# Performance work log

Hardware: AMD Instinct MI355X
Metric: run time of the kernel (lower is better)

Reference implementation:

```python
import jax, jax.numpy as jnp
import numpy as np
from jax.scipy.special import gammaln, xlogy

B, S, C = 2, 2048, 1536
H, DK, DV = 8, 64, 192
F_REL = C // H  # 192 relative-position features


def positional_features_all(positions, feature_size, seq_length):
    # positions: [1, 2S-1] float32 (signed relative distances)
    n = feature_size // 6  # basis per class per sign
    ap = jnp.abs(positions)  # [1, 2S-1]
    Sf = float(seq_length)
    # exponential decay features
    max_range = float(np.log(Sf) / np.log(2.0))
    half_life = 2.0 ** jnp.linspace(3.0, max_range, n)  # min_half_life = 3.0
    feat_exp = jnp.exp(-jnp.log(2.0) / half_life * ap[..., None])
    # central mask features
    center_widths = 2.0 ** jnp.arange(1, n + 1, dtype=jnp.float32) - 1.0
    feat_cm = (center_widths > ap[..., None]).astype(jnp.float32)
    # gamma pdf features
    stddev = Sf / (2.0 * n)
    start_mean = Sf / n
    mean = jnp.linspace(start_mean, Sf, n)
    conc = (mean / stddev) ** 2
    rate = mean / (stddev ** 2)
    xg = ap[..., None]
    log_unnorm = xlogy(conc - 1.0, xg) - rate * xg
    log_norm = gammaln(conc) - conc * jnp.log(rate)
    prob = jnp.exp(log_unnorm - log_norm) + 1e-8
    feat_g = prob / jnp.max(prob, axis=1, keepdims=True)
    emb = jnp.concatenate([feat_exp, feat_cm, feat_g], axis=-1)  # [1, 2S-1, 3n]
    emb = jnp.concatenate([emb, jnp.sign(positions)[..., None] * emb], axis=-1)
    return emb  # [1, 2S-1, feature_size]


def relative_shift(x):
    # x: [B, H, T, 2T-1] -> [B, H, T, T] (Transformer-XL shift trick)
    b, h, t, _ = x.shape
    x = jnp.pad(x, ((0, 0), (0, 0), (0, 0), (1, 0)))  # [B,H,T,2T]
    x = x.reshape(b, h, 2 * t, t)[:, :, 1:, :]          # [B,H,2T-1,T]
    x = x.reshape(b, h, t, 2 * t - 1)[:, :, :, :t]      # [B,H,T,T]
    return x


def setup_inputs() -> dict:
    key = jax.random.key(0)
    ks = jax.random.split(key, 8)
    inp = {
        "x": jax.random.normal(ks[0], (B, S, C), dtype=jnp.float32),
        "mask": jax.random.randint(ks[1], (B, S), 0, 2, dtype=jnp.int32),
        "Wq": jax.random.normal(ks[2], (C, H * DK), dtype=jnp.float32) * 0.02,
        "Wk": jax.random.normal(ks[3], (C, H * DK), dtype=jnp.float32) * 0.02,
        "Wv": jax.random.normal(ks[4], (C, H * DV), dtype=jnp.float32) * 0.02,
        "Wr": jax.random.normal(ks[5], (F_REL, H * DK), dtype=jnp.float32) * 0.02,
        "r_w_bias": jax.random.normal(ks[6], (1, H, 1, DK), dtype=jnp.float32) * 0.02,
        "Wo": jax.random.normal(ks[7], (H * DV, H * DV), dtype=jnp.float32) * 0.02,
        "bo": jnp.zeros((H * DV,), dtype=jnp.float32),
    }
    return inp


def reference(x, mask, Wq, Wk, Wv, Wr, r_w_bias, Wo, bo):
    b, s, c = x.shape
    # projections -> [B, H, S, d]
    q = (x @ Wq).reshape(b, s, H, DK).transpose(0, 2, 1, 3) * (DK ** -0.5)
    k = (x @ Wk).reshape(b, s, H, DK).transpose(0, 2, 1, 3)
    v = (x @ Wv).reshape(b, s, H, DV).transpose(0, 2, 1, 3)
    # relative positional encodings for distances -S+1 .. S-1
    dist = jnp.arange(-s + 1, s, dtype=jnp.float32)[None, :]  # [1, 2S-1]
    pe = positional_features_all(dist, F_REL, s)               # [1, 2S-1, F_REL]
    r_k = (pe[0] @ Wr).reshape(2 * s - 1, H, DK).transpose(1, 0, 2)  # [H, 2S-1, DK]
    # content + position logits
    content_logits = jnp.einsum('bhqd,bhkd->bhqk', q, k)                   # [B,H,S,S]
    rel_logits = jnp.einsum('bhqd,hkd->bhqk', q + r_w_bias, r_k)           # [B,H,S,2S-1]
    logits = content_logits + relative_shift(rel_logits)
    logits = jnp.where(mask[:, None, None, :] == 0, -1e9, logits)
    weights = jax.nn.softmax(logits, axis=-1)
    out = jnp.einsum('bhqk,bhkd->bhqd', weights, v)  # [B,H,S,DV]
    out = out.transpose(0, 2, 1, 3).reshape(b, s, H * DV)
    return out @ Wo + bo
```

## Files before the change

### kernel.cpp

```cpp
#include <hip/hip_runtime.h>
#include <math.h>

#define SEQ 2048
#define CDIM 1536
#define HN 8
#define DVC 192
#define BN 2
#define NPOS 4095
#define HDK 512
#define HDV 1536
#define PSTR 72

typedef __attribute__((ext_vector_type(8))) _Float16 hf8v;
typedef __attribute__((ext_vector_type(4))) _Float16 hf4v;
typedef __attribute__((ext_vector_type(4))) float f4v;

static __device__ __forceinline__ f4v mfma16(hf8v a, hf8v b, f4v c) {
  return __builtin_amdgcn_mfma_f32_16x16x32_f16(a, b, c, 0, 0, 0);
}
static __device__ __forceinline__ void gl2lds16(const void* g, void* l) {
  __builtin_amdgcn_global_load_lds((const __attribute__((address_space(1))) unsigned int*)g,
                                   (__attribute__((address_space(3))) unsigned int*)l,
                                   16, 0, 0);
}
static __device__ __forceinline__ float rowmax16(float x) {
  x = fmaxf(x, __int_as_float(__builtin_amdgcn_update_dpp(0, __float_as_int(x), 0x128, 0xf, 0xf, true)));
  x = fmaxf(x, __int_as_float(__builtin_amdgcn_update_dpp(0, __float_as_int(x), 0x124, 0xf, 0xf, true)));
  x = fmaxf(x, __int_as_float(__builtin_amdgcn_update_dpp(0, __float_as_int(x), 0x122, 0xf, 0xf, true)));
  x = fmaxf(x, __int_as_float(__builtin_amdgcn_update_dpp(0, __float_as_int(x), 0x121, 0xf, 0xf, true)));
  return x;
}

#define PF_B   512
#define CAST_B 6144
#define TWQ_B  768
#define TWK_B  768
#define TWV_B  2304
#define TWO_B  2304
#define TWR_B  96
#define PREP_BLOCKS (PF_B + CAST_B + TWQ_B + TWK_B + TWV_B + TWO_B + TWR_B)

__device__ __forceinline__ void twc_tile(const float* __restrict__ W, _Float16* __restrict__ WT,
                                         int K, int N, int tile, float (*tls)[33], int tid) {
  int ntn = N >> 5;
  int nt = tile % ntn, kt = tile / ntn;
  int k0 = kt * 32, n0 = nt * 32;
  int tx = tid & 31, ty = tid >> 5;
#pragma unroll
  for (int p = 0; p < 4; p++) tls[ty + p * 8][tx] = W[(size_t)(k0 + ty + p * 8) * N + n0 + tx];
  __syncthreads();
#pragma unroll
  for (int p = 0; p < 4; p++) {
    int n = ty + p * 8;
    WT[(size_t)(n0 + n) * K + k0 + tx] = (_Float16)tls[tx][n];
  }
}

__global__ __launch_bounds__(256) void prep_kernel(
    const float* __restrict__ x, const float* __restrict__ Wq, const float* __restrict__ Wk,
    const float* __restrict__ Wv, const float* __restrict__ Wo, const float* __restrict__ Wr,
    float* __restrict__ pe_raw, unsigned* __restrict__ gmax, _Float16* __restrict__ xb,
    _Float16* __restrict__ WTqkv, _Float16* __restrict__ WoT, _Float16* __restrict__ WrT) {
  __shared__ float tls[32][33];
  int blk = blockIdx.x, tid = threadIdx.x;
  if (blk < PF_B) {
    int j = blk >> 4;
    int pos = (blk & 15) * 256 + tid;
    float prob = 0.0f;
    if (pos < NPOS) {
      float ap = fabsf((float)(pos - (SEQ - 1)));
      float hl = exp2f(3.0f + 8.0f * (float)j / 31.0f);
      float fe = exp2f(-ap / hl);
      float cw = exp2f((float)(j + 1)) - 1.0f;
      float fc = (cw > ap) ? 1.0f : 0.0f;
      float conc = 4.0f * (float)((j + 1) * (j + 1));
      float rate = (float)(j + 1) / 16.0f;
      float log_norm = lgammaf(conc) - conc * logf(rate);
      float log_un = (conc - 1.0f) * logf(ap) - rate * ap;
      prob = expf(log_un - log_norm) + 1e-8f;
      pe_raw[pos * 96 + j] = fe;
      pe_raw[pos * 96 + 32 + j] = fc;
      pe_raw[pos * 96 + 64 + j] = prob;
    }
    float m = prob;
#pragma unroll
    for (int off = 32; off > 0; off >>= 1) m = fmaxf(m, __shfl_down(m, off));
    __shared__ float red[4];
    if ((tid & 63) == 0) red[tid >> 6] = m;
    __syncthreads();
    if (tid == 0) {
      m = fmaxf(fmaxf(red[0], red[1]), fmaxf(red[2], red[3]));
      atomicMax(&gmax[j], __float_as_uint(m));
    }
  } else if (blk < PF_B + CAST_B) {
    int i = ((blk - PF_B) * 256 + tid) * 4;
    float4 v = *(const float4*)(x + i);
    _Float16 o[4] = {(_Float16)v.x, (_Float16)v.y, (_Float16)v.z, (_Float16)v.w};
    *(unsigned long long*)(xb + i) = *(const unsigned long long*)o;
  } else if (blk < PF_B + CAST_B + TWQ_B) {
    twc_tile(Wq, WTqkv + 0 * (size_t)CDIM, CDIM, HDK, blk - (PF_B + CAST_B), tls, tid);
  } else if (blk < PF_B + CAST_B + TWQ_B + TWK_B) {
    twc_tile(Wk, WTqkv + 512 * (size_t)CDIM, CDIM, HDK, blk - (PF_B + CAST_B + TWQ_B), tls, tid);
  } else if (blk < PF_B + CAST_B + TWQ_B + TWK_B + TWV_B) {
    twc_tile(Wv, WTqkv + 1024 * (size_t)CDIM, CDIM, HDV, blk - (PF_B + CAST_B + TWQ_B + TWK_B), tls, tid);
  } else if (blk < PF_B + CAST_B + TWQ_B + TWK_B + TWV_B + TWO_B) {
    twc_tile(Wo, WoT, CDIM, HDV, blk - (PF_B + CAST_B + TWQ_B + TWK_B + TWV_B), tls, tid);
  } else {
    twc_tile(Wr, WrT, 192, HDK, blk - (PF_B + CAST_B + TWQ_B + TWK_B + TWV_B + TWO_B), tls, tid);
  }
}

__global__ __launch_bounds__(256) void pe_norm_kernel(const float* __restrict__ pe_raw,
                                                      const unsigned* __restrict__ gmax,
                                                      _Float16* __restrict__ pe_h) {
  int idx = blockIdx.x * 256 + threadIdx.x;
  int pos = idx / 96, f = idx - pos * 96;
  float val = 0.0f, sval = 0.0f;
  if (pos < NPOS) {
    val = pe_raw[pos * 96 + f];
    if (f >= 64) val *= 1.0f / __uint_as_float(gmax[f - 64]);
    float sgn = (pos > SEQ - 1) ? 1.0f : ((pos < SEQ - 1) ? -1.0f : 0.0f);
    sval = sgn * val;
  }
  pe_h[pos * 192 + f] = (_Float16)val;
  pe_h[pos * 192 + 96 + f] = (_Float16)sval;
}

template <int MODE>
__global__ __launch_bounds__(256, 2) void mfma_gemm(
    const _Float16* __restrict__ A, const _Float16* __restrict__ B,
    const float* __restrict__ bias, void* __restrict__ out0, void* __restrict__ out1,
    void* __restrict__ out2, int K) {
  __shared__ __align__(16) _Float16 As[128 * 64];
  __shared__ __align__(16) _Float16 Bs[128 * 64];
  const int tid = threadIdx.x;
  const int lane = tid & 63, l15 = lane & 15, quad = lane >> 4;
  const int wv = tid >> 6;
  const int wm = (wv & 1) * 64, wn = (wv >> 1) * 64;
  const int row0 = blockIdx.y * 128, col0 = blockIdx.x * 128;
  f4v acc[4][4];
#pragma unroll
  for (int i = 0; i < 4; i++)
#pragma unroll
    for (int j = 0; j < 4; j++) acc[i][j] = (f4v)0.0f;

  for (int k0 = 0; k0 < K; k0 += 64) {
    __syncthreads();
#pragma unroll
    for (int p = 0; p < 4; p++) {
      int idx = tid + p * 256;
      int rr = idx >> 3, sc = idx & 7;
      int gc = (sc ^ (rr & 7)) << 3;
      gl2lds16(A + (size_t)(row0 + rr) * K + k0 + gc, As + idx * 8);
      gl2lds16(B + (size_t)(col0 + rr) * K + k0 + gc, Bs + idx * 8);
    }
    __syncthreads();
    hf8v af[4][2], bfr[4][2];
#pragma unroll
    for (int t = 0; t < 4; t++) {
      int lrA = wm + t * 16 + l15;
      int lrB = wn + t * 16 + l15;
#pragma unroll
      for (int kc = 0; kc < 2; kc++) {
        af[t][kc]  = *(const hf8v*)(As + lrA * 64 + ((((kc << 2) | quad) ^ (lrA & 7)) << 3));
        bfr[t][kc] = *(const hf8v*)(Bs + lrB * 64 + ((((kc << 2) | quad) ^ (lrB & 7)) << 3));
      }
    }
#pragma unroll
    for (int kc = 0; kc < 2; kc++)
#pragma unroll
      for (int mt = 0; mt < 4; mt++)
#pragma unroll
        for (int nt = 0; nt < 4; nt++)
          acc[mt][nt] = mfma16(af[mt][kc], bfr[nt][kc], acc[mt][nt]);
  }
#pragma unroll
  for (int mt = 0; mt < 4; mt++)
#pragma unroll
    for (int reg = 0; reg < 4; reg++) {
      int r = row0 + wm + mt * 16 + quad * 4 + reg;
      int bb = r >> 11, ss = r & (SEQ - 1);
#pragma unroll
      for (int nt = 0; nt < 4; nt++) {
        int c = col0 + wn + nt * 16 + l15;
        float vv = acc[mt][nt][reg];
        if (MODE == 0) {
          if (c < 512) {
            ((_Float16*)out0)[(size_t)r * HDK + c] = (_Float16)(vv * 0.125f);
          } else if (c < 1024) {
            int cc = c - 512, h = cc >> 6, d = cc & 63;
            ((_Float16*)out1)[(((size_t)bb * HN + h) * SEQ + ss) * 64 + d] = (_Float16)vv;
          } else {
            int cc = c - 1024, h = cc / DVC, e = cc - h * DVC;
            int jp = (ss & ~63) | ((ss & 15) << 2) | ((ss >> 4) & 3);
            ((_Float16*)out2)[(((size_t)bb * HN + h) * DVC + e) * SEQ + jp] = (_Float16)vv;
          }
        } else if (MODE == 1) {
          int h = c >> 6, d = c & 63;
          ((_Float16*)out0)[((size_t)h * 4096 + r) * 64 + d] = (_Float16)vv;
        } else {
          ((float*)out0)[(size_t)r * HDV + c] = vv + bias[c];
        }
      }
    }
}

template <bool SPLITKV>
__global__ __launch_bounds__(256, 2) void attn_mfma(
    const _Float16* __restrict__ qb, const _Float16* __restrict__ kb,
    const _Float16* __restrict__ vtb, const _Float16* __restrict__ rkb,
    const float* __restrict__ rwb, const int* __restrict__ mask,
    _Float16* __restrict__ attn_out, float* __restrict__ Opart, float* __restrict__ ml) {
  __shared__ __align__(16) _Float16 Vts[192 * 64];
  __shared__ __align__(16) _Float16 RKs[192 * 64];
  __shared__ __align__(16) _Float16 Kts[64 * 64];
  __shared__ __align__(16) _Float16 Pbs[128 * PSTR];

  const int lin = blockIdx.x;
  const int chunk = SPLITKV ? 64 : 32;
  const int swz = (lin & 7) * chunk + (lin >> 3);
  const int bx = swz & 15;
  const int by = swz >> 4;
  const int i0 = bx * 128;
  const int bh = SPLITKV ? (by & 15) : by;
  const int half = SPLITKV ? (by >> 4) : 0;
  const int b = bh >> 3, h = bh & 7;
  const int tid = threadIdx.x;
  const int wv = tid >> 6, lane = tid & 63;
  const int l15 = lane & 15, quad = lane >> 4;

  hf8v qf[2][2], qbf[2][2];
#pragma unroll
  for (int s = 0; s < 2; s++) {
    int qrow = i0 + wv * 32 + s * 16 + l15;
    const _Float16* qp = qb + (size_t)(b * SEQ + qrow) * HDK + h * 64;
#pragma unroll
    for (int kc = 0; kc < 2; kc++) {
      hf8v qv = *(const hf8v*)(qp + kc * 32 + quad * 8);
      qf[s][kc] = qv;
      hf8v t;
#pragma unroll
      for (int j = 0; j < 8; j++)
        t[j] = (_Float16)((float)qv[j] + rwb[h * 64 + kc * 32 + quad * 8 + j]);
      qbf[s][kc] = t;
    }
  }

  f4v Of[2][12];
#pragma unroll
  for (int s = 0; s < 2; s++)
#pragma unroll
    for (int se = 0; se < 12; se++) Of[s][se] = (f4v)0.0f;
  float m_i[2][4] = {{-INFINITY, -INFINITY, -INFINITY, -INFINITY},
                     {-INFINITY, -INFINITY, -INFINITY, -INFINITY}};
  float l_i[2][4] = {{0.f, 0.f, 0.f, 0.f}, {0.f, 0.f, 0.f, 0.f}};

  const int j0beg = SPLITKV ? half * (SEQ / 2) : 0;
  const int j0end = SPLITKV ? j0beg + SEQ / 2 : SEQ;

  for (int j0 = j0beg; j0 < j0end; j0 += 64) {
    __syncthreads();
    int mraw[4];
#pragma unroll
    for (int st = 0; st < 4; st++) mraw[st] = mask[b * SEQ + j0 + st * 16 + l15];
    {
      const int U0 = j0 - i0 + 1920;
#pragma unroll
      for (int r = 0; r < 2; r++) {
        int idx = tid + r * 256, row = idx >> 3, sc = idx & 7;
        gl2lds16(kb + ((size_t)bh * SEQ + j0 + row) * 64 + ((sc ^ (row & 7)) << 3), Kts + idx * 8);
      }
#pragma unroll
      for (int r = 0; r < 6; r++) {
        int idx = tid + r * 256, row = idx >> 3, sc = idx & 7;
        gl2lds16(rkb + ((size_t)h * 4096 + U0 + row) * 64 + ((sc ^ (row & 7)) << 3), RKs + idx * 8);
      }
#pragma unroll
      for (int r = 0; r < 6; r++) {
        int idx = tid + r * 256, row = idx >> 3, sc = idx & 7;
        gl2lds16(vtb + ((size_t)bh * DVC + row) * SEQ + j0 + ((sc ^ (row & 7)) << 3), Vts + idx * 8);
      }
    }
    asm volatile("s_waitcnt vmcnt(6)" ::: "memory");
    __builtin_amdgcn_s_barrier();
    __builtin_amdgcn_sched_barrier(0);
    float mv[4];
#pragma unroll
    for (int st = 0; st < 4; st++) mv[st] = mraw[st] ? 0.f : -1e9f;

#pragma unroll
    for (int s = 0; s < 2; s++) {
      __builtin_amdgcn_s_setprio(1);
      f4v Sf[4];
#pragma unroll
      for (int st = 0; st < 4; st++) {
        Sf[st] = (f4v)0.0f;
#pragma unroll
        for (int kc = 0; kc < 2; kc++) {
          int row = st * 16 + l15;
          hf8v kf = *(const hf8v*)(Kts + row * 64 + ((((kc << 2) | quad) ^ (row & 7)) << 3));
          Sf[st] = mfma16(qf[s][kc], kf, Sf[st]);
        }
      }
      f4v Rf[5];
      const int tb = 112 - 32 * wv - 16 * s;
#pragma unroll
      for (int u = 0; u < 5; u++) {
        Rf[u] = (f4v)0.0f;
#pragma unroll
        for (int kc = 0; kc < 2; kc++) {
          int row = tb + u * 16 + l15;
          hf8v rf = *(const hf8v*)(RKs + row * 64 + ((((kc << 2) | quad) ^ (row & 7)) << 3));
          Rf[u] = mfma16(qbf[s][kc], rf, Rf[u]);
        }
      }
      __builtin_amdgcn_s_setprio(0);
#pragma unroll
      for (int reg = 0; reg < 4; reg++) {
        int delta = l15 - (quad << 2) - reg + 15;
        int srcl = (quad << 4) | (delta & 15);
        float sh0 = __shfl(Rf[0][reg], srcl, 64);
        float sh1 = __shfl(Rf[1][reg], srcl, 64);
        float sh2 = __shfl(Rf[2][reg], srcl, 64);
        float sh3 = __shfl(Rf[3][reg], srcl, 64);
        float sh4 = __shfl(Rf[4][reg], srcl, 64);
        bool hib = delta >= 16;
        Sf[0][reg] += (hib ? sh1 : sh0) + mv[0];
        Sf[1][reg] += (hib ? sh2 : sh1) + mv[1];
        Sf[2][reg] += (hib ? sh3 : sh2) + mv[2];
        Sf[3][reg] += (hib ? sh4 : sh3) + mv[3];
      }
#pragma unroll
      for (int reg = 0; reg < 4; reg++) {
        float t = fmaxf(fmaxf(Sf[0][reg], Sf[1][reg]), fmaxf(Sf[2][reg], Sf[3][reg]));
        t = rowmax16(t);
        if (__any(t - m_i[s][reg] > 8.0f)) {
          float mn = fmaxf(m_i[s][reg], t);
          float alpha = __expf(m_i[s][reg] - mn);
          m_i[s][reg] = mn;
          l_i[s][reg] *= alpha;
#pragma unroll
          for (int se = 0; se < 12; se++) Of[s][se][reg] *= alpha;
        }
        float mcur = m_i[s][reg];
        hf4v pv;
        float rs = 0.f;
#pragma unroll
        for (int st = 0; st < 4; st++) {
          float p = __expf(Sf[st][reg] - mcur);
          rs += p;
          pv[st] = (_Float16)p;
        }
        l_i[s][reg] += rs;
        *(hf4v*)(Pbs + (size_t)(wv * 32 + s * 16 + quad * 4 + reg) * PSTR + l15 * 4) = pv;
      }
    }

    hf8v pa[2][2];
#pragma unroll
    for (int s = 0; s < 2; s++)
#pragma unroll
      for (int kc = 0; kc < 2; kc++)
        pa[s][kc] = *(const hf8v*)(Pbs + (size_t)(wv * 32 + s * 16 + l15) * PSTR +
                                   kc * 32 + quad * 8);
    asm volatile("s_waitcnt vmcnt(0)" ::: "memory");
    __builtin_amdgcn_s_barrier();
    __builtin_amdgcn_sched_barrier(0);
    __builtin_amdgcn_s_setprio(1);
#pragma unroll
    for (int se = 0; se < 12; se++) {
#pragma unroll
      for (int kc = 0; kc < 2; kc++) {
        int row = se * 16 + l15;
        hf8v vf = *(const hf8v*)(Vts + row * 64 + ((((kc << 2) | quad) ^ (row & 7)) << 3));
        Of[0][se] = mfma16(pa[0][kc], vf, Of[0][se]);
        Of[1][se] = mfma16(pa[1][kc], vf, Of[1][se]);
      }
    }
    __builtin_amdgcn_s_setprio(0);
  }

#pragma unroll
  for (int s = 0; s < 2; s++)
#pragma unroll
    for (int reg = 0; reg < 4; reg++) {
      float ls = l_i[s][reg];
      ls += __shfl_xor(ls, 1);
      ls += __shfl_xor(ls, 2);
      ls += __shfl_xor(ls, 4);
      ls += __shfl_xor(ls, 8);
      int row = i0 + wv * 32 + s * 16 + quad * 4 + reg;
      int rg = b * SEQ + row;
      if constexpr (SPLITKV) {
        float* Op = Opart + ((size_t)(half * 4096 + rg)) * HDV + h * DVC;
#pragma unroll
        for (int se = 0; se < 12; se++) Op[se * 16 + l15] = Of[s][se][reg];
        if (l15 == 0) {
          size_t mlb = (((size_t)half * 4096 + rg) * HN + h) * 2;
          ml[mlb] = m_i[s][reg];
          ml[mlb + 1] = ls;
        }
      } else {
        float inv = 1.0f / ls;
        size_t base2 = (size_t)rg * HDV + h * DVC;
#pragma unroll
        for (int se = 0; se < 12; se++)
          attn_out[base2 + se * 16 + l15] = (_Float16)(Of[s][se][reg] * inv);
      }
    }
}

__global__ __launch_bounds__(256) void combine_kernel(const float* __restrict__ Opart,
                                                      const float* __restrict__ ml,
                                                      _Float16* __restrict__ attn_out) {
  int i4 = blockIdx.x * 256 + threadIdx.x;
  int rg = i4 / 384, c4 = (i4 - rg * 384) * 4;
  int h = c4 / DVC;
  size_t mlb0 = ((size_t)rg * HN + h) * 2;
  size_t mlb1 = (((size_t)4096 + rg) * HN + h) * 2;
  float m0 = ml[mlb0], l0 = ml[mlb0 + 1];
  float m1 = ml[mlb1], l1 = ml[mlb1 + 1];
  float M = fmaxf(m0, m1);
  float w0 = __expf(m0 - M), w1 = __expf(m1 - M);
  float inv = 1.0f / (l0 * w0 + l1 * w1);
  float4 O0 = *(const float4*)(Opart + (size_t)rg * HDV + c4);
  float4 O1 = *(const float4*)(Opart + ((size_t)4096 + rg) * HDV + c4);
  _Float16 o[4] = {(_Float16)((O0.x * w0 + O1.x * w1) * inv),
                   (_Float16)((O0.y * w0 + O1.y * w1) * inv),
                   (_Float16)((O0.z * w0 + O1.z * w1) * inv),
                   (_Float16)((O0.w * w0 + O1.w * w1) * inv)};
  *(unsigned long long*)(attn_out + (size_t)rg * HDV + c4) = *(const unsigned long long*)o;
}

extern "C" void kernel_launch(void* const* d_in, const int* in_sizes, int n_in,
                              void* d_out, int out_size, void* d_ws, size_t ws_size,
                              hipStream_t stream) {
  const float* x    = (const float*)d_in[0];
  const int*   mask = (const int*)d_in[1];
  const float* Wq   = (const float*)d_in[2];
  const float* Wk   = (const float*)d_in[3];
  const float* Wv   = (const float*)d_in[4];
  const float* Wr   = (const float*)d_in[5];
  const float* rwb  = (const float*)d_in[6];
  const float* Wo   = (const float*)d_in[7];
  const float* bo   = (const float*)d_in[8];
  float* out = (float*)d_out;

  char* wsb = (char*)d_ws;
  size_t o = 0;
  auto al = [](size_t v) { return (v + 255) & ~(size_t)255; };
#define CARVE(ptr_t, name, bytes) ptr_t name = (ptr_t)(wsb + o); o = al(o + (bytes));
  CARVE(float*, pe_raw, (size_t)4096 * 96 * 4)
  CARVE(unsigned*, gmax, 128)
  CARVE(_Float16*, pe_h, (size_t)4096 * 192 * 2)
  CARVE(_Float16*, WrT, (size_t)HDK * 192 * 2)
  CARVE(_Float16*, xb, (size_t)BN * SEQ * CDIM * 2)
  CARVE(_Float16*, WTqkv, (size_t)2560 * CDIM * 2)
  CARVE(_Float16*, WoT, (size_t)HDV * CDIM * 2)
  CARVE(_Float16*, qb, (size_t)BN * SEQ * HDK * 2)
  CARVE(_Float16*, kb, (size_t)BN * SEQ * HDK * 2)
  CARVE(_Float16*, vtb, (size_t)BN * SEQ * HDV * 2)
  CARVE(_Float16*, rkb, (size_t)HN * 4096 * 64 * 2)
  _Float16* attnh = xb;
  CARVE(float*, Opart, (size_t)2 * 4096 * HDV * 4)
  CARVE(float*, ml, (size_t)2 * 4096 * HN * 2 * 4)
  bool dosplit = (o <= ws_size);

  hipMemsetAsync(gmax, 0, 32 * sizeof(unsigned), stream);
  prep_kernel<<<PREP_BLOCKS, 256, 0, stream>>>(x, Wq, Wk, Wv, Wo, Wr, pe_raw, gmax, xb,
                                               WTqkv, WoT, WrT);
  pe_norm_kernel<<<4096 * 96 / 256, 256, 0, stream>>>(pe_raw, gmax, pe_h);
  mfma_gemm<0><<<dim3(2560 / 128, BN * SEQ / 128), 256, 0, stream>>>(
      xb, WTqkv, nullptr, qb, kb, vtb, CDIM);
  mfma_gemm<1><<<dim3(HDK / 128, 4096 / 128), 256, 0, stream>>>(
      pe_h, WrT, nullptr, rkb, nullptr, nullptr, 192);
  if (dosplit) {
    attn_mfma<true><<<512, 256, 0, stream>>>(qb, kb, vtb, rkb, rwb, mask,
                                             attnh, Opart, ml);
    combine_kernel<<<4096 * 384 / 256, 256, 0, stream>>>(Opart, ml, attnh);
  } else {
    attn_mfma<false><<<256, 256, 0, stream>>>(qb, kb, vtb, rkb, rwb, mask,
                                              attnh, nullptr, nullptr);
  }
  mfma_gemm<2><<<dim3(HDV / 128, BN * SEQ / 128), 256, 0, stream>>>(
      attnh, WoT, bo, out, nullptr, nullptr, CDIM);
}
```

Before: 316.8 us.

## Split attention block into 8 waves with 16 query rows each

The attention kernel now runs 512 threads (8 waves) per block instead of 256. Each wave handles 16 query rows instead of 32, so per-thread accumulator and Q registers are halved, and the K/RK/V tile loads are shared across twice as many threads. The aim is more resident waves and better latency hiding. In exchange each V and RK fragment read from LDS feeds only one MFMA instead of two, which raises LDS traffic per FLOP, and barriers now synchronise more waves.

```diff
diff --git a/kernel.cpp b/kernel.cpp
--- a/kernel.cpp
+++ b/kernel.cpp
@@ -206,7 +206,7 @@
 }
 
 template <bool SPLITKV>
-__global__ __launch_bounds__(256, 2) void attn_mfma(
+__global__ __launch_bounds__(512, 4) void attn_mfma(
     const _Float16* __restrict__ qb, const _Float16* __restrict__ kb,
     const _Float16* __restrict__ vtb, const _Float16* __restrict__ rkb,
     const float* __restrict__ rwb, const int* __restrict__ mask,
@@ -229,31 +229,27 @@
   const int wv = tid >> 6, lane = tid & 63;
   const int l15 = lane & 15, quad = lane >> 4;
 
-  hf8v qf[2][2], qbf[2][2];
-#pragma unroll
-  for (int s = 0; s < 2; s++) {
-    int qrow = i0 + wv * 32 + s * 16 + l15;
+  hf8v qf[2], qbf[2];
+  {
+    int qrow = i0 + wv * 16 + l15;
     const _Float16* qp = qb + (size_t)(b * SEQ + qrow) * HDK + h * 64;
 #pragma unroll
     for (int kc = 0; kc < 2; kc++) {
       hf8v qv = *(const hf8v*)(qp + kc * 32 + quad * 8);
-      qf[s][kc] = qv;
+      qf[kc] = qv;
       hf8v t;
 #pragma unroll
       for (int j = 0; j < 8; j++)
         t[j] = (_Float16)((float)qv[j] + rwb[h * 64 + kc * 32 + quad * 8 + j]);
-      qbf[s][kc] = t;
-    }
-  }
-
-  f4v Of[2][12];
-#pragma unroll
-  for (int s = 0; s < 2; s++)
-#pragma unroll
-    for (int se = 0; se < 12; se++) Of[s][se] = (f4v)0.0f;
-  float m_i[2][4] = {{-INFINITY, -INFINITY, -INFINITY, -INFINITY},
-                     {-INFINITY, -INFINITY, -INFINITY, -INFINITY}};
-  float l_i[2][4] = {{0.f, 0.f, 0.f, 0.f}, {0.f, 0.f, 0.f, 0.f}};
+      qbf[kc] = t;
+    }
+  }
+
+  f4v Of[12];
+#pragma unroll
+  for (int se = 0; se < 12; se++) Of[se] = (f4v)0.0f;
+  float m_i[4] = {-INFINITY, -INFINITY, -INFINITY, -INFINITY};
+  float l_i[4] = {0.f, 0.f, 0.f, 0.f};
 
   const int j0beg = SPLITKV ? half * (SEQ / 2) : 0;
   const int j0end = SPLITKV ? j0beg + SEQ / 2 : SEQ;
@@ -265,104 +261,97 @@
     for (int st = 0; st < 4; st++) mraw[st] = mask[b * SEQ + j0 + st * 16 + l15];
     {
       const int U0 = j0 - i0 + 1920;
-#pragma unroll
-      for (int r = 0; r < 2; r++) {
-        int idx = tid + r * 256, row = idx >> 3, sc = idx & 7;
-        gl2lds16(kb + ((size_t)bh * SEQ + j0 + row) * 64 + ((sc ^ (row & 7)) << 3), Kts + idx * 8);
-      }
-#pragma unroll
-      for (int r = 0; r < 6; r++) {
-        int idx = tid + r * 256, row = idx >> 3, sc = idx & 7;
+      {
+        int row = tid >> 3, sc = tid & 7;
+        gl2lds16(kb + ((size_t)bh * SEQ + j0 + row) * 64 + ((sc ^ (row & 7)) << 3), Kts + tid * 8);
+      }
+#pragma unroll
+      for (int r = 0; r < 3; r++) {
+        int idx = tid + r * 512, row = idx >> 3, sc = idx & 7;
         gl2lds16(rkb + ((size_t)h * 4096 + U0 + row) * 64 + ((sc ^ (row & 7)) << 3), RKs + idx * 8);
       }
 #pragma unroll
-      for (int r = 0; r < 6; r++) {
-        int idx = tid + r * 256, row = idx >> 3, sc = idx & 7;
+      for (int r = 0; r < 3; r++) {
+        int idx = tid + r * 512, row = idx >> 3, sc = idx & 7;
         gl2lds16(vtb + ((size_t)bh * DVC + row) * SEQ + j0 + ((sc ^ (row & 7)) << 3), Vts + idx * 8);
       }
     }
-    asm volatile("s_waitcnt vmcnt(6)" ::: "memory");
+    asm volatile("s_waitcnt vmcnt(3)" ::: "memory");
     __builtin_amdgcn_s_barrier();
     __builtin_amdgcn_sched_barrier(0);
     float mv[4];
 #pragma unroll
     for (int st = 0; st < 4; st++) mv[st] = mraw[st] ? 0.f : -1e9f;
 
-#pragma unroll
-    for (int s = 0; s < 2; s++) {
-      __builtin_amdgcn_s_setprio(1);
-      f4v Sf[4];
+    __builtin_amdgcn_s_setprio(1);
+    f4v Sf[4];
+#pragma unroll
+    for (int st = 0; st < 4; st++) {
+      Sf[st] = (f4v)0.0f;
+#pragma unroll
+      for (int kc = 0; kc < 2; kc++) {
+        int row = st * 16 + l15;
+        hf8v kf = *(const hf8v*)(Kts + row * 64 + ((((kc << 2) | quad) ^ (row & 7)) << 3));
+        Sf[st] = mfma16(qf[kc], kf, Sf[st]);
+      }
+    }
+    f4v Rf[5];
+    const int tb = 112 - 16 * wv;
+#pragma unroll
+    for (int u = 0; u < 5; u++) {
+      Rf[u] = (f4v)0.0f;
+#pragma unroll
+      for (int kc = 0; kc < 2; kc++) {
+        int row = tb + u * 16 + l15;
+        hf8v rf = *(const hf8v*)(RKs + row * 64 + ((((kc << 2) | quad) ^ (row & 7)) << 3));
+        Rf[u] = mfma16(qbf[kc], rf, Rf[u]);
+      }
+    }
+    __builtin_amdgcn_s_setprio(0);
+#pragma unroll
+    for (int reg = 0; reg < 4; reg++) {
+      int delta = l15 - (quad << 2) - reg + 15;
+      int srcl = (quad << 4) | (delta & 15);
+      float sh0 = __shfl(Rf[0][reg], srcl, 64);
+      float sh1 = __shfl(Rf[1][reg], srcl, 64);
+      float sh2 = __shfl(Rf[2][reg], srcl, 64);
+      float sh3 = __shfl(Rf[3][reg], srcl, 64);
+      float sh4 = __shfl(Rf[4][reg], srcl, 64);
+      bool hib = delta >= 16;
+      Sf[0][reg] += (hib ? sh1 : sh0) + mv[0];
+      Sf[1][reg] += (hib ? sh2 : sh1) + mv[1];
+      Sf[2][reg] += (hib ? sh3 : sh2) + mv[2];
+      Sf[3][reg] += (hib ? sh4 : sh3) + mv[3];
+    }
+#pragma unroll
+    for (int reg = 0; reg < 4; reg++) {
+      float t = fmaxf(fmaxf(Sf[0][reg], Sf[1][reg]), fmaxf(Sf[2][reg], Sf[3][reg]));
+      t = rowmax16(t);
+      if (__any(t - m_i[reg] > 8.0f)) {
+        float mn = fmaxf(m_i[reg], t);
+        float alpha = __expf(m_i[reg] - mn);
+        m_i[reg] = mn;
+        l_i[reg] *= alpha;
+#pragma unroll
+        for (int se = 0; se < 12; se++) Of[se][reg] *= alpha;
+      }
+      float mcur = m_i[reg];
+      hf4v pv;
+      float rs = 0.f;
 #pragma unroll
       for (int st = 0; st < 4; st++) {
-        Sf[st] = (f4v)0.0f;
-#pragma unroll
-        for (int kc = 0; kc < 2; kc++) {
-          int row = st * 16 + l15;
-          hf8v kf = *(const hf8v*)(Kts + row * 64 + ((((kc << 2) | quad) ^ (row & 7)) << 3));
-          Sf[st] = mfma16(qf[s][kc], kf, Sf[st]);
-        }
-      }
-      f4v Rf[5];
-      const int tb = 112 - 32 * wv - 16 * s;
-#pragma unroll
-      for (int u = 0; u < 5; u++) {
-        Rf[u] = (f4v)0.0f;
-#pragma unroll
-        for (int kc = 0; kc < 2; kc++) {
-          int row = tb + u * 16 + l15;
-          hf8v rf = *(const hf8v*)(RKs + row * 64 + ((((kc << 2) | quad) ^ (row & 7)) << 3));
-          Rf[u] = mfma16(qbf[s][kc], rf, Rf[u]);
-        }
-      }
-      __builtin_amdgcn_s_setprio(0);
-#pragma unroll
-      for (int reg = 0; reg < 4; reg++) {
-        int delta = l15 - (quad << 2) - reg + 15;
-        int srcl = (quad << 4) | (delta & 15);
-        float sh0 = __shfl(Rf[0][reg], srcl, 64);
-        float sh1 = __shfl(Rf[1][reg], srcl, 64);
-        float sh2 = __shfl(Rf[2][reg], srcl, 64);
-        float sh3 = __shfl(Rf[3][reg], srcl, 64);
-        float sh4 = __shfl(Rf[4][reg], srcl, 64);
-        bool hib = delta >= 16;
-        Sf[0][reg] += (hib ? sh1 : sh0) + mv[0];
-        Sf[1][reg] += (hib ? sh2 : sh1) + mv[1];
-        Sf[2][reg] += (hib ? sh3 : sh2) + mv[2];
-        Sf[3][reg] += (hib ? sh4 : sh3) + mv[3];
-      }
-#pragma unroll
-      for (int reg = 0; reg < 4; reg++) {
-        float t = fmaxf(fmaxf(Sf[0][reg], Sf[1][reg]), fmaxf(Sf[2][reg], Sf[3][reg]));
-        t = rowmax16(t);
-        if (__any(t - m_i[s][reg] > 8.0f)) {
-          float mn = fmaxf(m_i[s][reg], t);
-          float alpha = __expf(m_i[s][reg] - mn);
-          m_i[s][reg] = mn;
-          l_i[s][reg] *= alpha;
-#pragma unroll
-          for (int se = 0; se < 12; se++) Of[s][se][reg] *= alpha;
-        }
-        float mcur = m_i[s][reg];
-        hf4v pv;
-        float rs = 0.f;
-#pragma unroll
-        for (int st = 0; st < 4; st++) {
-          float p = __expf(Sf[st][reg] - mcur);
-          rs += p;
-          pv[st] = (_Float16)p;
-        }
-        l_i[s][reg] += rs;
-        *(hf4v*)(Pbs + (size_t)(wv * 32 + s * 16 + quad * 4 + reg) * PSTR + l15 * 4) = pv;
-      }
-    }
-
-    hf8v pa[2][2];
-#pragma unroll
-    for (int s = 0; s < 2; s++)
-#pragma unroll
-      for (int kc = 0; kc < 2; kc++)
-        pa[s][kc] = *(const hf8v*)(Pbs + (size_t)(wv * 32 + s * 16 + l15) * PSTR +
-                                   kc * 32 + quad * 8);
+        float p = __expf(Sf[st][reg] - mcur);
+        rs += p;
+        pv[st] = (_Float16)p;
+      }
+      l_i[reg] += rs;
+      *(hf4v*)(Pbs + (size_t)(wv * 16 + quad * 4 + reg) * PSTR + l15 * 4) = pv;
+    }
+
+    hf8v pa[2];
+#pragma unroll
+    for (int kc = 0; kc < 2; kc++)
+      pa[kc] = *(const hf8v*)(Pbs + (size_t)(wv * 16 + l15) * PSTR + kc * 32 + quad * 8);
     asm volatile("s_waitcnt vmcnt(0)" ::: "memory");
     __builtin_amdgcn_s_barrier();
     __builtin_amdgcn_sched_barrier(0);
@@ -373,41 +362,38 @@
       for (int kc = 0; kc < 2; kc++) {
         int row = se * 16 + l15;
         hf8v vf = *(const hf8v*)(Vts + row * 64 + ((((kc << 2) | quad) ^ (row & 7)) << 3));
-        Of[0][se] = mfma16(pa[0][kc], vf, Of[0][se]);
-        Of[1][se] = mfma16(pa[1][kc], vf, Of[1][se]);
+        Of[se] = mfma16(pa[kc], vf, Of[se]);
       }
     }
     __builtin_amdgcn_s_setprio(0);
   }
 
 #pragma unroll
-  for (int s = 0; s < 2; s++)
-#pragma unroll
-    for (int reg = 0; reg < 4; reg++) {
-      float ls = l_i[s][reg];
-      ls += __shfl_xor(ls, 1);
-      ls += __shfl_xor(ls, 2);
-      ls += __shfl_xor(ls, 4);
-      ls += __shfl_xor(ls, 8);
-      int row = i0 + wv * 32 + s * 16 + quad * 4 + reg;
-      int rg = b * SEQ + row;
-      if constexpr (SPLITKV) {
-        float* Op = Opart + ((size_t)(half * 4096 + rg)) * HDV + h * DVC;
-#pragma unroll
-        for (int se = 0; se < 12; se++) Op[se * 16 + l15] = Of[s][se][reg];
-        if (l15 == 0) {
-          size_t mlb = (((size_t)half * 4096 + rg) * HN + h) * 2;
-          ml[mlb] = m_i[s][reg];
-          ml[mlb + 1] = ls;
-        }
-      } else {
-        float inv = 1.0f / ls;
-        size_t base2 = (size_t)rg * HDV + h * DVC;
-#pragma unroll
-        for (int se = 0; se < 12; se++)
-          attn_out[base2 + se * 16 + l15] = (_Float16)(Of[s][se][reg] * inv);
-      }
-    }
+  for (int reg = 0; reg < 4; reg++) {
+    float ls = l_i[reg];
+    ls += __shfl_xor(ls, 1);
+    ls += __shfl_xor(ls, 2);
+    ls += __shfl_xor(ls, 4);
+    ls += __shfl_xor(ls, 8);
+    int row = i0 + wv * 16 + quad * 4 + reg;
+    int rg = b * SEQ + row;
+    if constexpr (SPLITKV) {
+      float* Op = Opart + ((size_t)(half * 4096 + rg)) * HDV + h * DVC;
+#pragma unroll
+      for (int se = 0; se < 12; se++) Op[se * 16 + l15] = Of[se][reg];
+      if (l15 == 0) {
+        size_t mlb = (((size_t)half * 4096 + rg) * HN + h) * 2;
+        ml[mlb] = m_i[reg];
+        ml[mlb + 1] = ls;
+      }
+    } else {
+      float inv = 1.0f / ls;
+      size_t base2 = (size_t)rg * HDV + h * DVC;
+#pragma unroll
+      for (int se = 0; se < 12; se++)
+        attn_out[base2 + se * 16 + l15] = (_Float16)(Of[se][reg] * inv);
+    }
+  }
 }
 
 __global__ __launch_bounds__(256) void combine_kernel(const float* __restrict__ Opart,
@@ -475,11 +461,11 @@
   mfma_gemm<1><<<dim3(HDK / 128, 4096 / 128), 256, 0, stream>>>(
       pe_h, WrT, nullptr, rkb, nullptr, nullptr, 192);
   if (dosplit) {
-    attn_mfma<true><<<512, 256, 0, stream>>>(qb, kb, vtb, rkb, rwb, mask,
+    attn_mfma<true><<<512, 512, 0, stream>>>(qb, kb, vtb, rkb, rwb, mask,
                                              attnh, Opart, ml);
     combine_kernel<<<4096 * 384 / 256, 256, 0, stream>>>(Opart, ml, attnh);
   } else {
-    attn_mfma<false><<<256, 256, 0, stream>>>(qb, kb, vtb, rkb, rwb, mask,
+    attn_mfma<false><<<256, 512, 0, stream>>>(qb, kb, vtb, rkb, rwb, mask,
                                               attnh, nullptr, nullptr);
   }
   mfma_gemm<2><<<dim3(HDV / 128, BN * SEQ / 128), 256, 0, stream>>>(
```

New measurement: 355.1 us. +12.1%, slower.
